# Optimization experiments

Hardware: AMD Instinct MI355X
Metric: run time of the kernel (lower is better)

## Reference

```python
import jax, jax.numpy as jnp
import numpy as np

START_IDX = 1  # module-level constant assumed in original repo
PAD_IDX = 0

B, T, V, E, H, F, HW = 32, 128, 16000, 512, 1024, 2048, 7


def setup_inputs() -> dict:
    key = jax.random.key(0)
    ks = jax.random.split(key, 11)
    s = 0.02
    emb = jax.random.normal(ks[2], (V, E), jnp.float32) * s
    emb = emb.at[PAD_IDX].set(0.0)  # padding_idx row is zero
    return {
        "features": jax.random.normal(ks[0], (B, F, HW, HW), jnp.float32),
        "reports": jax.random.randint(ks[1], (B, T), 0, V, jnp.int32),
        "fc_W": jax.random.normal(ks[3], (2 * H, F), jnp.float32) * s,
        "fc_b": jax.random.normal(ks[4], (2 * H,), jnp.float32) * s,
        "emb": emb,
        "W_ih": jax.random.normal(ks[5], (4 * H, E), jnp.float32) * s,
        "W_hh": jax.random.normal(ks[6], (4 * H, H), jnp.float32) * s,
        "b_ih": jax.random.normal(ks[7], (4 * H,), jnp.float32) * s,
        "b_hh": jax.random.normal(ks[8], (4 * H,), jnp.float32) * s,
        "Wv": jax.random.normal(ks[9], (V, H), jnp.float32) * s,
        "bv": jax.random.normal(ks[10], (V,), jnp.float32) * s,
    }


def reference(features, reports, fc_W, fc_b, emb, W_ih, W_hh, b_ih, b_hh, Wv, bv):
    # features_fc: AdaptiveAvgPool2d((1,1)) -> Flatten -> Linear(F, 2H)
    pooled = features.mean(axis=(2, 3))                      # [B, F]
    init = pooled @ fc_W.T + fc_b                            # [B, 2H]
    h0, c0 = init[:, :H], init[:, H:]

    # teacher forcing: step 0 uses START_IDX, step t uses reports[:, t-1]
    start = jnp.full((reports.shape[0], 1), START_IDX, dtype=reports.dtype)
    in_idx = jnp.concatenate([start, reports[:, :-1]], axis=1)  # [B, T]
    x = emb[in_idx]                                             # [B, T, E]

    def step(carry, x_t):
        h, c = carry
        gates = x_t @ W_ih.T + b_ih + h @ W_hh.T + b_hh        # [B, 4H]
        i, f, g, o = jnp.split(gates, 4, axis=-1)
        c = jax.nn.sigmoid(f) * c + jax.nn.sigmoid(i) * jnp.tanh(g)
        h = jax.nn.sigmoid(o) * jnp.tanh(c)
        return (h, c), h

    _, hs = jax.lax.scan(step, (h0, c0), jnp.swapaxes(x, 0, 1))  # [T, B, H]
    hs = jnp.swapaxes(hs, 0, 1)                                  # [B, T, H]
    seq_out = jnp.einsum("bth,vh->btv", hs, Wv) + bv             # [B, T, V]
    return (seq_out,)
```

## Files before the change

### kernel.cpp

```cpp
#include <hip/hip_runtime.h>
#include <hip/hip_bf16.h>
#include <stdint.h>

#define BB 32
#define TT 128
#define VV 16000
#define EE 512
#define HH 1024
#define FF 2048
#define NBLK 64

typedef __attribute__((ext_vector_type(8))) short short8;
typedef __attribute__((ext_vector_type(4))) float floatx4;

static __device__ __forceinline__ float bf2f(ushort u) {
    union { unsigned int i; float f; } v; v.i = ((unsigned int)u) << 16; return v.f;
}
static __device__ __forceinline__ ushort f2bf(float f) {
    union { float f; unsigned int i; } v; v.f = f;
    unsigned int x = v.i;
    return (ushort)((x + 0x7fffu + ((x >> 16) & 1u)) >> 16);
}
static __device__ __forceinline__ float sigf(float x) {
    return 1.0f / (1.0f + __expf(-x));
}

static __device__ __forceinline__ short8 ld8(const char* p, int f32) {
    if (f32) {
        const float4 a = *(const float4*)p;
        const float4 b = *(const float4*)(p + 16);
        short8 r;
        r[0] = (short)f2bf(a.x); r[1] = (short)f2bf(a.y);
        r[2] = (short)f2bf(a.z); r[3] = (short)f2bf(a.w);
        r[4] = (short)f2bf(b.x); r[5] = (short)f2bf(b.y);
        r[6] = (short)f2bf(b.z); r[7] = (short)f2bf(b.w);
        return r;
    }
    return *(const short8*)p;
}
static __device__ __forceinline__ float ldsc(const char* b, int i, int f32) {
    return f32 ? ((const float*)b)[i] : bf2f(((const ushort*)b)[i]);
}

__global__ void detect_kernel(const ushort* __restrict__ w, int* __restrict__ flag) {
    if (threadIdx.x == 0 && blockIdx.x == 0) {
        int cnt = 0;
        for (int i = 0; i < 512; i += 2) {
            ushort u = w[i];
            float x = bf2f(u);
            float ax = x < 0.f ? -x : x;
            if (u == 0u || u == 0x8000u || ax > 100.f) cnt++;
        }
        *flag = (cnt >= 8) ? 1 : 0;
    }
}

__global__ void conv_kernel(const char* __restrict__ in, ushort* __restrict__ out,
                            int n, const int* __restrict__ flagp) {
    int i = blockIdx.x * 256 + threadIdx.x;
    if (i >= n) return;
    int fl = *flagp;
    out[i] = fl ? f2bf(((const float*)in)[i]) : ((const ushort*)in)[i];
}

__global__ void pool_kernel(const char* __restrict__ feats, ushort* __restrict__ pooled,
                            const int* __restrict__ flagp) {
    int p = blockIdx.x * 256 + threadIdx.x;
    int fl = *flagp;
    float s = 0.f;
    if (fl) {
        const float* src = (const float*)feats + (size_t)p * 49;
        #pragma unroll
        for (int i = 0; i < 49; i++) s += src[i];
    } else {
        const ushort* src = (const ushort*)feats + (size_t)p * 49;
        #pragma unroll
        for (int i = 0; i < 49; i++) s += bf2f(src[i]);
    }
    pooled[p] = f2bf(s * (1.0f / 49.0f));
}

__global__ void h0prep_kernel(const ushort* __restrict__ initb, ushort* __restrict__ hb,
                              unsigned int* __restrict__ barcnt) {
    int i = blockIdx.x * 256 + threadIdx.x;
    int b = i >> 10, j = i & 1023;
    hb[i] = initb[b * 2048 + j];
    if (i == 0)
        __hip_atomic_store(barcnt, 0u, __ATOMIC_RELAXED, __HIP_MEMORY_SCOPE_AGENT);
}

__global__ void ridx_kernel(const int* __restrict__ reports, int* __restrict__ ridx) {
    int row = blockIdx.x * 256 + threadIdx.x;
    int b = row & 31, t = row >> 5;
    ridx[row] = (t == 0) ? 1 : reports[b * TT + t - 1];
}

__global__ __launch_bounds__(256) void gemm_bf16(
    const char* __restrict__ A, const char* __restrict__ Bm,
    const int* __restrict__ ridx,
    const char* __restrict__ bias1, const char* __restrict__ bias2,
    char* __restrict__ C, int M, int N, int K,
    const int* __restrict__ flagp, int aext, int bext, int oext, int swapxy)
{
    __shared__ ushort As[128 * 32];
    __shared__ ushort Bs[128 * 32];
    const int fl = *flagp;
    const int af32 = aext & fl, bf32 = bext & fl;
    const size_t eA = af32 ? 4 : 2, eB = bf32 ? 4 : 2;

    const int tid  = threadIdx.x;
    const int wave = tid >> 6, lane = tid & 63;
    const int ln = lane & 15, quad = lane >> 4;
    const int wm = wave & 1, wn = wave >> 1;
    const int bm = swapxy ? blockIdx.x : blockIdx.y;
    const int bn = swapxy ? blockIdx.y : blockIdx.x;

    floatx4 acc[4][4] = {};

    const int c0 = tid, c1 = 256 + tid;
    int lr0 = bm * 128 + (c0 >> 2); if (lr0 >= M) lr0 = M - 1;
    int lr1 = bm * 128 + (c1 >> 2); if (lr1 >= M) lr1 = M - 1;
    const int rA0 = ridx ? ridx[lr0] : lr0;
    const int rA1 = ridx ? ridx[lr1] : lr1;
    const int rB0 = bn * 128 + (c0 >> 2);
    const int rB1 = bn * 128 + (c1 >> 2);
    const char* gA0 = A  + ((size_t)rA0 * K + (c0 & 3) * 8) * eA;
    const char* gA1 = A  + ((size_t)rA1 * K + (c1 & 3) * 8) * eA;
    const char* gB0 = Bm + ((size_t)rB0 * K + (c0 & 3) * 8) * eB;
    const char* gB1 = Bm + ((size_t)rB1 * K + (c1 & 3) * 8) * eB;

    for (int k0 = 0; k0 < K; k0 += 32) {
        short8 va0 = ld8(gA0 + (size_t)k0 * eA, af32);
        short8 va1 = ld8(gA1 + (size_t)k0 * eA, af32);
        short8 vb0 = ld8(gB0 + (size_t)k0 * eB, bf32);
        short8 vb1 = ld8(gB1 + (size_t)k0 * eB, bf32);
        __syncthreads();
        *(short8*)(As + c0 * 8) = va0;
        *(short8*)(As + c1 * 8) = va1;
        *(short8*)(Bs + c0 * 8) = vb0;
        *(short8*)(Bs + c1 * 8) = vb1;
        __syncthreads();

        short8 af[4], bfg[4];
        #pragma unroll
        for (int i = 0; i < 4; i++)
            af[i] = *(const short8*)(As + (wm * 64 + i * 16 + ln) * 32 + quad * 8);
        #pragma unroll
        for (int i = 0; i < 4; i++)
            bfg[i] = *(const short8*)(Bs + (wn * 64 + i * 16 + ln) * 32 + quad * 8);
        #pragma unroll
        for (int i = 0; i < 4; i++)
            #pragma unroll
            for (int j = 0; j < 4; j++)
                acc[i][j] = __builtin_amdgcn_mfma_f32_16x16x32_bf16(af[i], bfg[j], acc[i][j], 0, 0, 0);
    }

    const int of32 = oext & fl;
    const int col_base = bn * 128 + wn * 64;
    const int row_base = bm * 128 + wm * 64;
    #pragma unroll
    for (int j = 0; j < 4; j++) {
        const int col = col_base + j * 16 + ln;
        float bb = ldsc(bias1, col, fl);
        if (bias2) bb += ldsc(bias2, col, fl);
        #pragma unroll
        for (int i = 0; i < 4; i++) {
            const int row0 = row_base + i * 16 + quad * 4;
            #pragma unroll
            for (int r = 0; r < 4; r++) {
                const int row = row0 + r;
                if (row < M) {
                    float v = acc[i][j][r] + bb;
                    if (of32) ((float*)C)[(size_t)row * N + col] = v;
                    else      ((ushort*)C)[(size_t)row * N + col] = f2bf(v);
                }
            }
        }
    }
}

__global__ __launch_bounds__(512, 2) void lstm_kernel(
    const ushort* __restrict__ Whhb,
    const ushort* __restrict__ gx,
    const ushort* __restrict__ initb,
    ushort* __restrict__ hbuf,
    ushort* __restrict__ hs,
    unsigned int* __restrict__ barcnt)
{
    __shared__ ushort hsm[32 * 1024];
    __shared__ float pbuf[8][32][17];

    const int jb = blockIdx.x;
    const int tid = threadIdx.x;
    const int w = tid >> 6;
    const int lane = tid & 63;
    const int ln = lane & 15, quad = lane >> 4;
    const int s = w >> 1, q = w & 1;

    short8 wf[16];
    {
        const ushort* wb = Whhb + (size_t)(s * 1024 + jb * 16 + ln) * HH + q * 512 + quad * 8;
        #pragma unroll
        for (int kc = 0; kc < 16; kc++)
            wf[kc] = *(const short8*)(wb + kc * 32);
    }

    const int cb = tid >> 4, hc = tid & 15;
    const int hcol = jb * 16 + hc;
    float creg = bf2f(initb[(size_t)cb * 2048 + 1024 + hcol]);

    #pragma unroll 1
    for (int t = 0; t < TT; t++) {
        float gxv[4];
        {
            const ushort* gp = gx + ((size_t)t * BB + cb) * 4096 + hcol;
            #pragma unroll
            for (int g = 0; g < 4; g++) gxv[g] = bf2f(gp[g * 1024]);
        }

        if (t > 0) {
            if (tid == 0) {
                const unsigned target = (unsigned)(NBLK * t);
                while (__hip_atomic_load(barcnt, __ATOMIC_RELAXED,
                                         __HIP_MEMORY_SCOPE_AGENT) < target)
                    __builtin_amdgcn_s_sleep(1);
            }
            __syncthreads();
            asm volatile("" ::: "memory");
        }

        {
            const ushort* hp = hbuf + (size_t)(t & 1) * BB * HH;
            unsigned long long v[16];
            #pragma unroll
            for (int j = 0; j < 16; j++) {
                const int c = tid + 512 * j;
                v[j] = __hip_atomic_load((const unsigned long long*)hp + c,
                                         __ATOMIC_RELAXED, __HIP_MEMORY_SCOPE_AGENT);
            }
            #pragma unroll
            for (int j = 0; j < 16; j++) {
                const int c = tid + 512 * j;
                const int row = c >> 8;
                const int inb = (c & 255) * 8;
                *(unsigned long long*)((char*)hsm + row * 2048 + (inb ^ ((row & 7) << 4))) = v[j];
            }
        }
        __syncthreads();

        floatx4 acc0 = {}, acc1 = {};
        {
            const char* base0 = (const char*)hsm + ln * 2048;
            const char* base1 = (const char*)hsm + (16 + ln) * 2048;
            const int x0 = (ln & 7) << 4, x1 = ((16 + ln) & 7) << 4;
            #pragma unroll
            for (int kc = 0; kc < 16; kc++) {
                const int inb = (q * 512 + kc * 32 + quad * 8) * 2;
                short8 a0 = *(const short8*)(base0 + (inb ^ x0));
                short8 a1 = *(const short8*)(base1 + (inb ^ x1));
                acc0 = __builtin_amdgcn_mfma_f32_16x16x32_bf16(a0, wf[kc], acc0, 0, 0, 0);
                acc1 = __builtin_amdgcn_mfma_f32_16x16x32_bf16(a1, wf[kc], acc1, 0, 0, 0);
            }
        }
        #pragma unroll
        for (int r = 0; r < 4; r++) {
            pbuf[w][quad * 4 + r][ln]      = acc0[r];
            pbuf[w][16 + quad * 4 + r][ln] = acc1[r];
        }
        __syncthreads();

        {
            float gv[4];
            #pragma unroll
            for (int g = 0; g < 4; g++)
                gv[g] = pbuf[2 * g][cb][hc] + pbuf[2 * g + 1][cb][hc] + gxv[g];
            creg = sigf(gv[1]) * creg + sigf(gv[0]) * tanhf(gv[2]);
            const float hn = sigf(gv[3]) * tanhf(creg);
            unsigned hv = (unsigned)f2bf(hn);
            unsigned up = (unsigned)__shfl_down((int)hv, 1);
            if ((hc & 1) == 0) {
                const unsigned pk = hv | (up << 16);
                ushort* hnx = hbuf + (size_t)((t + 1) & 1) * BB * HH;
                __hip_atomic_store((unsigned*)(hnx + (size_t)cb * HH + hcol), pk,
                                   __ATOMIC_RELAXED, __HIP_MEMORY_SCOPE_AGENT);
                __hip_atomic_store((unsigned*)(hs + ((size_t)cb * TT + t) * HH + hcol), pk,
                                   __ATOMIC_RELAXED, __HIP_MEMORY_SCOPE_AGENT);
            }
        }

        __builtin_amdgcn_fence(__ATOMIC_RELEASE, "agent");
        __syncthreads();
        if (tid == 0)
            __hip_atomic_fetch_add(barcnt, 1u, __ATOMIC_RELAXED, __HIP_MEMORY_SCOPE_AGENT);
    }
}

extern "C" void kernel_launch(void* const* d_in, const int* in_sizes, int n_in,
                              void* d_out, int out_size, void* d_ws, size_t ws_size,
                              hipStream_t stream) {
    const char* feats   = (const char*)d_in[0];
    const int*  reports = (const int*) d_in[1];
    const char* fcW     = (const char*)d_in[2];
    const char* fcb     = (const char*)d_in[3];
    const char* emb     = (const char*)d_in[4];
    const char* Wih     = (const char*)d_in[5];
    const char* Whh     = (const char*)d_in[6];
    const char* bih     = (const char*)d_in[7];
    const char* bhh     = (const char*)d_in[8];
    const char* Wv      = (const char*)d_in[9];
    const char* bv      = (const char*)d_in[10];

    char* p = (char*)d_ws;
    ushort* gx     = (ushort*)p; p += (size_t)BB * TT * 4096 * 2;
    ushort* hs     = (ushort*)p; p += (size_t)BB * TT * HH * 2;
    ushort* Whhb   = (ushort*)p; p += (size_t)4096 * HH * 2;
    ushort* pooled = (ushort*)p; p += (size_t)BB * FF * 2;
    ushort* initb  = (ushort*)p; p += (size_t)BB * 2048 * 2;
    ushort* hbuf   = (ushort*)p; p += (size_t)2 * BB * HH * 2;
    int*    ridx   = (int*)   p; p += (size_t)BB * TT * 4;
    int*    flag   = (int*)   p; p += 16;
    unsigned int* barcnt = (unsigned int*)p; p += 16;

    detect_kernel<<<1, 64, 0, stream>>>((const ushort*)fcW, flag);
    conv_kernel  <<<16384, 256, 0, stream>>>(Whh, Whhb, 4096 * HH, flag);
    pool_kernel  <<<256, 256, 0, stream>>>(feats, pooled, flag);
    ridx_kernel  <<<16,  256, 0, stream>>>(reports, ridx);

    gemm_bf16<<<dim3(16, 1), 256, 0, stream>>>((const char*)pooled, fcW, nullptr,
                                               fcb, nullptr, (char*)initb,
                                               32, 2048, 2048, flag, 0, 1, 0, 0);
    h0prep_kernel<<<128, 256, 0, stream>>>(initb, hbuf, barcnt);
    gemm_bf16<<<dim3(32, 32), 256, 0, stream>>>(emb, Wih, ridx, bih, bhh,
                                                (char*)gx, BB * TT, 4096, EE,
                                                flag, 1, 1, 0, 1);

    {
        const ushort* a0 = Whhb; const ushort* a1 = gx; const ushort* a2 = initb;
        ushort* a3 = hbuf; ushort* a4 = hs; unsigned int* a5 = barcnt;
        void* kargs[] = { (void*)&a0, (void*)&a1, (void*)&a2,
                          (void*)&a3, (void*)&a4, (void*)&a5 };
        hipLaunchCooperativeKernel(lstm_kernel, dim3(NBLK), dim3(512), kargs, 0, stream);
    }

    gemm_bf16<<<dim3(32, 125), 256, 0, stream>>>((const char*)hs, Wv, nullptr,
                                                 bv, nullptr, (char*)d_out,
                                                 BB * TT, VV, HH, flag, 0, 1, 1, 1);
}
```

Before: 2.229 ms.

## Replace LSTM counter barrier with per-block flags and add LDS-direct output GEMM

```diff
diff --git a/kernel.cpp b/kernel.cpp
--- a/kernel.cpp
+++ b/kernel.cpp
@@ -23,6 +23,12 @@
 }
 static __device__ __forceinline__ float sigf(float x) {
     return 1.0f / (1.0f + __expf(-x));
+}
+
+static __device__ __forceinline__ void gload_lds16(const void* g, void* l) {
+    __builtin_amdgcn_global_load_lds(
+        (const __attribute__((address_space(1))) unsigned int*)g,
+        (__attribute__((address_space(3))) unsigned int*)l, 16, 0, 0);
 }
 
 static __device__ __forceinline__ short8 ld8(const char* p, int f32) {
@@ -81,12 +87,12 @@
 }
 
 __global__ void h0prep_kernel(const ushort* __restrict__ initb, ushort* __restrict__ hb,
-                              unsigned int* __restrict__ barcnt) {
+                              unsigned int* __restrict__ flags) {
     int i = blockIdx.x * 256 + threadIdx.x;
     int b = i >> 10, j = i & 1023;
     hb[i] = initb[b * 2048 + j];
-    if (i == 0)
-        __hip_atomic_store(barcnt, 0u, __ATOMIC_RELAXED, __HIP_MEMORY_SCOPE_AGENT);
+    if (i < NBLK)
+        __hip_atomic_store(flags + i, 0u, __ATOMIC_RELAXED, __HIP_MEMORY_SCOPE_AGENT);
 }
 
 __global__ void ridx_kernel(const int* __restrict__ reports, int* __restrict__ ridx) {
@@ -179,13 +185,89 @@
     }
 }
 
+__global__ __launch_bounds__(256) void gemm_bf16_fast(
+    const ushort* __restrict__ A, const ushort* __restrict__ Bm,
+    const char* __restrict__ bias,
+    char* __restrict__ C, int M, int N, int K,
+    const int* __restrict__ flagp, int oext, int gx_, int gy_)
+{
+    __shared__ ushort As[128 * 32];
+    __shared__ ushort Bs[128 * 32];
+    const int fl = *flagp;
+
+    const int tid  = threadIdx.x;
+    const int wave = tid >> 6, lane = tid & 63;
+    const int ln = lane & 15, quad = lane >> 4;
+    const int wm = wave & 1, wn = wave >> 1;
+
+    const int nwg = gx_ * gy_;
+    const int L   = blockIdx.y * gx_ + blockIdx.x;
+    const int wg  = (L % 8) * (nwg / 8) + L / 8;
+    const int bm  = wg % gx_;
+    const int bn  = wg / gx_;
+
+    floatx4 acc[4][4] = {};
+
+    const int c0 = tid, c1 = 256 + tid;
+    const ushort* gA0 = A  + (size_t)(bm * 128 + (c0 >> 2)) * K + (c0 & 3) * 8;
+    const ushort* gA1 = A  + (size_t)(bm * 128 + (c1 >> 2)) * K + (c1 & 3) * 8;
+    const ushort* gB0 = Bm + (size_t)(bn * 128 + (c0 >> 2)) * K + (c0 & 3) * 8;
+    const ushort* gB1 = Bm + (size_t)(bn * 128 + (c1 >> 2)) * K + (c1 & 3) * 8;
+    ushort* lA0 = As + (wave * 64) * 8;
+    ushort* lA1 = As + (256 + wave * 64) * 8;
+    ushort* lB0 = Bs + (wave * 64) * 8;
+    ushort* lB1 = Bs + (256 + wave * 64) * 8;
+
+    for (int k0 = 0; k0 < K; k0 += 32) {
+        __syncthreads();
+        gload_lds16(gA0 + k0, lA0);
+        gload_lds16(gA1 + k0, lA1);
+        gload_lds16(gB0 + k0, lB0);
+        gload_lds16(gB1 + k0, lB1);
+        __syncthreads();
+
+        short8 af[4], bfg[4];
+        #pragma unroll
+        for (int i = 0; i < 4; i++)
+            af[i] = *(const short8*)(As + (wm * 64 + i * 16 + ln) * 32 + quad * 8);
+        #pragma unroll
+        for (int i = 0; i < 4; i++)
+            bfg[i] = *(const short8*)(Bs + (wn * 64 + i * 16 + ln) * 32 + quad * 8);
+        #pragma unroll
+        for (int i = 0; i < 4; i++)
+            #pragma unroll
+            for (int j = 0; j < 4; j++)
+                acc[i][j] = __builtin_amdgcn_mfma_f32_16x16x32_bf16(af[i], bfg[j], acc[i][j], 0, 0, 0);
+    }
+
+    const int of32 = oext & fl;
+    const int col_base = bn * 128 + wn * 64;
+    const int row_base = bm * 128 + wm * 64;
+    #pragma unroll
+    for (int j = 0; j < 4; j++) {
+        const int col = col_base + j * 16 + ln;
+        const float bb = ldsc(bias, col, fl);
+        #pragma unroll
+        for (int i = 0; i < 4; i++) {
+            const int row0 = row_base + i * 16 + quad * 4;
+            #pragma unroll
+            for (int r = 0; r < 4; r++) {
+                const int row = row0 + r;
+                float v = acc[i][j][r] + bb;
+                if (of32) ((float*)C)[(size_t)row * N + col] = v;
+                else      ((ushort*)C)[(size_t)row * N + col] = f2bf(v);
+            }
+        }
+    }
+}
+
 __global__ __launch_bounds__(512, 2) void lstm_kernel(
     const ushort* __restrict__ Whhb,
     const ushort* __restrict__ gx,
     const ushort* __restrict__ initb,
     ushort* __restrict__ hbuf,
     ushort* __restrict__ hs,
-    unsigned int* __restrict__ barcnt)
+    unsigned int* __restrict__ flags)
 {
     __shared__ ushort hsm[32 * 1024];
     __shared__ float pbuf[8][32][17];
@@ -219,13 +301,11 @@
         }
 
         if (t > 0) {
-            if (tid == 0) {
-                const unsigned target = (unsigned)(NBLK * t);
-                while (__hip_atomic_load(barcnt, __ATOMIC_RELAXED,
-                                         __HIP_MEMORY_SCOPE_AGENT) < target)
-                    __builtin_amdgcn_s_sleep(1);
-            }
-            __syncthreads();
+            while (true) {
+                unsigned v = __hip_atomic_load(flags + lane, __ATOMIC_RELAXED,
+                                               __HIP_MEMORY_SCOPE_AGENT);
+                if (__all((int)(v >= (unsigned)t))) break;
+            }
             asm volatile("" ::: "memory");
         }
 
@@ -283,15 +363,15 @@
                 ushort* hnx = hbuf + (size_t)((t + 1) & 1) * BB * HH;
                 __hip_atomic_store((unsigned*)(hnx + (size_t)cb * HH + hcol), pk,
                                    __ATOMIC_RELAXED, __HIP_MEMORY_SCOPE_AGENT);
-                __hip_atomic_store((unsigned*)(hs + ((size_t)cb * TT + t) * HH + hcol), pk,
-                                   __ATOMIC_RELAXED, __HIP_MEMORY_SCOPE_AGENT);
+                *(unsigned*)(hs + ((size_t)cb * TT + t) * HH + hcol) = pk;
             }
         }
 
         __builtin_amdgcn_fence(__ATOMIC_RELEASE, "agent");
         __syncthreads();
         if (tid == 0)
-            __hip_atomic_fetch_add(barcnt, 1u, __ATOMIC_RELAXED, __HIP_MEMORY_SCOPE_AGENT);
+            __hip_atomic_store(flags + jb, (unsigned)(t + 1), __ATOMIC_RELAXED,
+                               __HIP_MEMORY_SCOPE_AGENT);
     }
 }
 
@@ -319,7 +399,7 @@
     ushort* hbuf   = (ushort*)p; p += (size_t)2 * BB * HH * 2;
     int*    ridx   = (int*)   p; p += (size_t)BB * TT * 4;
     int*    flag   = (int*)   p; p += 16;
-    unsigned int* barcnt = (unsigned int*)p; p += 16;
+    unsigned int* flags = (unsigned int*)p; p += NBLK * 4;
 
     detect_kernel<<<1, 64, 0, stream>>>((const ushort*)fcW, flag);
     conv_kernel  <<<16384, 256, 0, stream>>>(Whh, Whhb, 4096 * HH, flag);
@@ -329,20 +409,23 @@
     gemm_bf16<<<dim3(16, 1), 256, 0, stream>>>((const char*)pooled, fcW, nullptr,
                                                fcb, nullptr, (char*)initb,
                                                32, 2048, 2048, flag, 0, 1, 0, 0);
-    h0prep_kernel<<<128, 256, 0, stream>>>(initb, hbuf, barcnt);
+    h0prep_kernel<<<128, 256, 0, stream>>>(initb, hbuf, flags);
     gemm_bf16<<<dim3(32, 32), 256, 0, stream>>>(emb, Wih, ridx, bih, bhh,
                                                 (char*)gx, BB * TT, 4096, EE,
                                                 flag, 1, 1, 0, 1);
 
     {
         const ushort* a0 = Whhb; const ushort* a1 = gx; const ushort* a2 = initb;
-        ushort* a3 = hbuf; ushort* a4 = hs; unsigned int* a5 = barcnt;
+        ushort* a3 = hbuf; ushort* a4 = hs; unsigned int* a5 = flags;
         void* kargs[] = { (void*)&a0, (void*)&a1, (void*)&a2,
                           (void*)&a3, (void*)&a4, (void*)&a5 };
         hipLaunchCooperativeKernel(lstm_kernel, dim3(NBLK), dim3(512), kargs, 0, stream);
     }
 
-    gemm_bf16<<<dim3(32, 125), 256, 0, stream>>>((const char*)hs, Wv, nullptr,
-                                                 bv, nullptr, (char*)d_out,
-                                                 BB * TT, VV, HH, flag, 0, 1, 1, 1);
-}
+    ushort* Wvb = gx;
+    conv_kernel<<<64000, 256, 0, stream>>>(Wv, Wvb, VV * HH, flag);
+    gemm_bf16_fast<<<dim3(32, 125), 256, 0, stream>>>((const ushort*)hs, Wvb,
+                                                      bv, (char*)d_out,
+                                                      BB * TT, VV, HH, flag,
+                                                      1, 32, 125);
+}
```

New measurement: 2.181 ms. 2.2% less time.
